# Kernel tuning notes

Measured on AMD Instinct MI355X. Metric: run time of the kernel, lower is better.

Reference implementation:

```python
import jax, jax.numpy as jnp
import numpy as np
import math

N = 50000      # nodes (single node type 'mapping_var')
D = 128        # in_feats
R = 3          # relations
E = 800000     # edges per relation
OUT = 64
ALPHA = 0.5
BETA1 = math.log(2.0)    # log(lambda/layer + 1), layer=1, lambda=1
BETA2 = math.log(1.5)    # layer=2
SLOPE = 0.01             # leaky_relu default negative slope


def setup_inputs() -> dict:
    key = jax.random.key(0)
    ks = jax.random.split(key, 8)
    x = jax.random.normal(ks[0], (N, D), dtype=jnp.float32)
    src = jax.random.randint(ks[1], (R, E), 0, N, dtype=jnp.int32)
    dst = jax.random.randint(ks[2], (R, E), 0, N, dtype=jnp.int32)
    W1 = jax.random.normal(ks[3], (R, D, D), dtype=jnp.float32) * 0.05
    b1 = jnp.zeros((R, D), dtype=jnp.float32)
    W2 = jax.random.normal(ks[4], (R, D, D), dtype=jnp.float32) * 0.05
    b2 = jnp.zeros((R, D), dtype=jnp.float32)
    Wlin = jax.random.normal(ks[5], (D, OUT), dtype=jnp.float32) * 0.05
    blin = jnp.zeros((OUT,), dtype=jnp.float32)
    return {"x": x, "src": src, "dst": dst, "W1": W1, "b1": b1,
            "W2": W2, "b2": b2, "Wlin": Wlin, "blin": blin}


def _gcn2_rel(h, feat0, src, dst, W, b, beta, act):
    """One GCN2Conv on one relation. h,feat0: [N,D]; src,dst: [E]."""
    ones = jnp.ones(src.shape, h.dtype)
    deg_out = jnp.maximum(jax.ops.segment_sum(ones, src, num_segments=N), 1.0)
    deg_in = jnp.maximum(jax.ops.segment_sum(ones, dst, num_segments=N), 1.0)
    hs = h * (deg_out ** -0.5)[:, None]              # src-side normalize
    agg = jax.ops.segment_sum(hs[src], dst, num_segments=N)  # SpMM via gather+scatter
    feat = agg * (deg_in ** -0.5)[:, None]           # dst-side normalize
    rst = feat * (1.0 - ALPHA) + ALPHA * feat0       # initial-residual blend
    rst = (1.0 - beta) * rst + beta * (rst @ W) + b  # identity mapping (project_initial_features)
    if act:
        rst = jnp.where(rst >= 0, rst, SLOPE * rst)  # leaky_relu
    return rst


def reference(x, src, dst, W1, b1, W2, b2, Wlin, blin):
    # conv1: per-relation GCN2Conv(layer=1, leaky_relu), mean-aggregate over relations
    h1 = jax.vmap(lambda s, d, w, bb: _gcn2_rel(x, x, s, d, w, bb, BETA1, True))(
        src, dst, W1, b1).mean(axis=0)
    # dropout: eval-mode identity
    # conv2: per-relation GCN2Conv(layer=2, no activation), feat_0 = original inputs
    h2 = jax.vmap(lambda s, d, w, bb: _gcn2_rel(h1, x, s, d, w, bb, BETA2, False))(
        src, dst, W2, b2).mean(axis=0)
    return h2 @ Wlin + blin
```

## Files before the change

### kernel.cpp

```cpp
#include <hip/hip_runtime.h>

#define NN    50000
#define DD    128
#define RR    3
#define EE    800000
#define OUTD  64
#define BKT   128
#define NBK   391
#define CAP   2560
#define CAPB  2560
#define CHUNK 8192
#define NCH   98
#define NPB   3125
#define SETUPB 6250
#define MCB   49
#define PGB   391
#define P64B  3125
#define ALPHA_ 0.5f
#define SLOPE_ 0.01f
#define BETA1_ 0.6931471805599453f
#define BETA2_ 0.4054651081081644f

typedef __attribute__((ext_vector_type(8))) short short8;
typedef __attribute__((ext_vector_type(4))) float f32x4;
typedef __attribute__((ext_vector_type(4))) unsigned int u32x4;

__device__ __forceinline__ unsigned short f2b(float f) {
    unsigned int u = __builtin_bit_cast(unsigned int, f);
    u += 0x7FFFu + ((u >> 16) & 1u);
    return (unsigned short)(u >> 16);
}
__device__ __forceinline__ unsigned int pack2(float lo, float hi) {
    return (unsigned int)f2b(lo) | ((unsigned int)f2b(hi) << 16);
}
__device__ __forceinline__ float blo(unsigned int w) { return __builtin_bit_cast(float, w << 16); }
__device__ __forceinline__ float bhi(unsigned int w) { return __builtin_bit_cast(float, w & 0xFFFF0000u); }

__global__ __launch_bounds__(256) void bin_kernel(
    const int* __restrict__ src, const int* __restrict__ dst,
    int* __restrict__ bcnt_d, int* __restrict__ bcnt_s,
    int* __restrict__ pairs_d, unsigned short* __restrict__ pairs_s)
{
    __shared__ int hist[NBK];
    __shared__ int lbase[NBK];
    __shared__ int gdelta[NBK];
    __shared__ int lcur[NBK];
    __shared__ unsigned int staging[CHUNK];
    unsigned short* staging16 = (unsigned short*)staging;
    const int tid = threadIdx.x;
    const int blk = blockIdx.x;
    const int phase = (blk >= RR * NCH);
    const int rb = phase ? blk - RR * NCH : blk;
    const int r = rb / NCH;
    const int chunk = rb % NCH;
    const int e0 = chunk * CHUNK;
    const int n = min(CHUNK, EE - e0);
    const int* sp = src + (size_t)r * EE + e0;
    const int* dp = dst + (size_t)r * EE + e0;
    const int* kp = phase ? sp : dp;

    for (int i = tid; i < NBK; i += 256) hist[i] = 0;
    __syncthreads();
    for (int i = tid; i < n; i += 256)
        atomicAdd(&hist[kp[i] >> 7], 1);
    __syncthreads();
    if (tid < 64) {
        int carry = 0;
        for (int c0 = 0; c0 < NBK; c0 += 64) {
            const int idx = c0 + tid;
            const int v = (idx < NBK) ? hist[idx] : 0;
            int incl = v;
            #pragma unroll
            for (int d = 1; d < 64; d <<= 1) {
                const int t = __shfl_up(incl, d, 64);
                if (tid >= d) incl += t;
            }
            if (idx < NBK) lbase[idx] = carry + incl - v;
            carry += __shfl(incl, 63, 64);
        }
    }
    __syncthreads();
    if (!phase) {
        for (int b = tid; b < NBK; b += 256) {
            lcur[b] = lbase[b];
            const int h = hist[b];
            if (h > 0) {
                const int gstart = (r * NBK + b) * CAP + atomicAdd(&bcnt_d[r * NBK + b], h);
                gdelta[b] = gstart - lbase[b];
            }
        }
        __syncthreads();
        for (int i = tid; i < n; i += 256) {
            const int d = dp[i];
            const int b = d >> 7;
            const int pos = atomicAdd(&lcur[b], 1);
            staging[pos] = (unsigned int)sp[i] | ((unsigned int)(d & 127) << 16)
                         | ((unsigned int)b << 23);
        }
        __syncthreads();
        for (int j = tid; j < n; j += 256) {
            const unsigned int v = staging[j];
            const int b = v >> 23;
            const int gi = gdelta[b] + j;
            const int lo = gi - (r * NBK + b) * CAP;
            if (lo < CAP) pairs_d[gi] = (int)(v & 0x7FFFFF);
        }
    } else {
        for (int b = tid; b < NBK; b += 256) {
            lcur[b] = lbase[b];
            const int h = hist[b];
            if (h > 0) {
                const int gstart = (r * NBK + b) * CAPB + atomicAdd(&bcnt_s[r * NBK + b], h);
                gdelta[b] = gstart - lbase[b];
            }
        }
        __syncthreads();
        for (int i = tid; i < n; i += 256) {
            const int s = sp[i];
            const int b = s >> 7;
            const int pos = atomicAdd(&lcur[b], 1);
            staging16[pos] = (unsigned short)((b << 7) | (s & 127));
        }
        __syncthreads();
        for (int j = tid; j < n; j += 256) {
            const unsigned short v = staging16[j];
            const int b = v >> 7;
            const int gi = gdelta[b] + j;
            const int lo = gi - (r * NBK + b) * CAPB;
            if (lo < CAPB) pairs_s[gi] = v;
        }
    }
}

__global__ __launch_bounds__(256) void dego_setup_kernel(
    const unsigned short* __restrict__ pairs_s, const int* __restrict__ bcnt_s,
    float* __restrict__ dego_r,
    const float* __restrict__ x, unsigned short* __restrict__ xb,
    const float* __restrict__ W1, const float* __restrict__ W2,
    const float* __restrict__ Wlin, unsigned short* __restrict__ Wt1,
    unsigned short* __restrict__ Wt2, unsigned short* __restrict__ WlT,
    const float* __restrict__ b2, const float* __restrict__ blin,
    unsigned short* __restrict__ MT, float* __restrict__ Cbuf)
{
    __shared__ int scnt[BKT];
    const int tid = threadIdx.x;
    const int blk = blockIdx.x;
    if (blk < RR * NBK) {
        const int n2 = min(bcnt_s[blk], CAPB);
        const unsigned short* ps = pairs_s + (size_t)blk * CAPB;
        if (tid < BKT) scnt[tid] = 0;
        __syncthreads();
        for (int i = tid; i < n2; i += 256)
            atomicAdd(&scnt[ps[i] & 127], 1);
        __syncthreads();
        if (tid < BKT) {
            const int r = blk / NBK;
            const int g = (blk % NBK) * BKT + tid;
            if (g < NN)
                dego_r[r * NN + g] = rsqrtf((float)max(scnt[tid], 1));
        }
    } else if (blk < RR * NBK + SETUPB) {
        const int i = (blk - RR * NBK) * 256 + tid;
        {
            const float4 v = ((const float4*)x)[i];
            ushort4 o;
            o.x = f2b(v.x); o.y = f2b(v.y); o.z = f2b(v.z); o.w = f2b(v.w);
            ((ushort4*)xb)[i] = o;
        }
        if (i < RR * DD * DD) {
            const int r = i >> 14, rem = i & 16383, nn = rem >> 7, k = rem & 127;
            const float diag = (k == nn) ? 1.0f : 0.0f;
            const float w1 = W1[r * DD * DD + k * DD + nn];
            Wt1[i] = f2b(BETA1_ * w1 + diag * (1.0f - BETA1_));
            const float w2 = W2[r * DD * DD + k * DD + nn];
            Wt2[i] = f2b((BETA2_ * w2 + diag * (1.0f - BETA2_)) * (1.0f / 3.0f));
        } else if (i < RR * DD * DD + OUTD * DD) {
            const int j = i - RR * DD * DD;
            const int nn = j >> 7, k = j & 127;
            WlT[j] = f2b(Wlin[k * OUTD + nn]);
        }
    } else {
        const int mb = blk - RR * NBK - SETUPB;
        if (mb < MCB - 1) {
            const int base = (mb * 256 + tid) * 2;
            #pragma unroll
            for (int ii = 0; ii < 2; ++ii) {
                const int gidx = base + ii;
                const int r = gidx >> 13;
                const int rem = gidx & 8191;
                const int o = rem >> 7, k = rem & 127;
                float s = 0.f;
                for (int nn = 0; nn < DD; ++nn)
                    s += W2[r * DD * DD + k * DD + nn] * Wlin[nn * OUTD + o];
                MT[gidx] = f2b((BETA2_ / 3.0f) * s + ((1.0f - BETA2_) / 3.0f) * Wlin[k * OUTD + o]);
            }
        } else {
            if (tid < OUTD) {
                float s = blin[tid];
                for (int nn = 0; nn < DD; ++nn) {
                    const float mb2 = (b2[nn] + b2[DD + nn] + b2[2 * DD + nn]) * (1.0f / 3.0f);
                    s += mb2 * Wlin[nn * OUTD + tid];
                }
                Cbuf[tid] = s;
            }
        }
    }
}

__global__ __launch_bounds__(256) void sort_kernel(
    int* __restrict__ pairs_d, const int* __restrict__ bcnt_d,
    const float* __restrict__ dego_r,
    int* __restrict__ off_g, int* __restrict__ cnt_g, float* __restrict__ degi_r)
{
    __shared__ int stage[CAP];
    __shared__ int cnt[BKT];
    __shared__ int base[BKT];
    __shared__ int pos[BKT];
    const int tid = threadIdx.x;
    const int bid = blockIdx.x;
    const int rr = bid / NBK;
    const int n = min(bcnt_d[bid], CAP);
    int* pp = pairs_d + (size_t)bid * CAP;
    const float* dego = dego_r + (size_t)rr * NN;
    if (tid < BKT) cnt[tid] = 0;
    __syncthreads();
    for (int i = tid; i < n; i += 256) {
        const int p = pp[i];
        stage[i] = p;
        atomicAdd(&cnt[p >> 16], 1);
    }
    __syncthreads();
    if (tid < 64) {
        int carry = 0;
        for (int c0 = 0; c0 < BKT; c0 += 64) {
            const int v = cnt[c0 + tid];
            int incl = v;
            #pragma unroll
            for (int d = 1; d < 64; d <<= 1) {
                const int t = __shfl_up(incl, d, 64);
                if (tid >= d) incl += t;
            }
            base[c0 + tid] = carry + incl - v;
            carry += __shfl(incl, 63, 64);
        }
    }
    __syncthreads();
    if (tid < BKT) {
        pos[tid] = base[tid];
        const int g = (bid % NBK) * BKT + tid;
        if (g < NN) {
            off_g[rr * NN + g] = bid * CAP + base[tid];
            cnt_g[rr * NN + g] = cnt[tid];
            degi_r[rr * NN + g] = rsqrtf((float)max(cnt[tid], 1));
        }
    }
    __syncthreads();
    for (int i = tid; i < n; i += 256) {
        const int p = stage[i];
        const int q = atomicAdd(&pos[p >> 16], 1);
        const int s = p & 0xFFFF;
        pp[q] = s | ((int)f2b(dego[s]) << 16);
    }
}

__global__ __launch_bounds__(256) void pull_all_kernel(
    const unsigned short* __restrict__ hb,
    const unsigned short* __restrict__ xb,
    const int* __restrict__ csrw, const int* __restrict__ off_g,
    const int* __restrict__ cnt_g, const float* __restrict__ degi_r,
    unsigned short* __restrict__ aggb)
{
    const int blk = blockIdx.x;
    const int r = blk / NPB;
    const int node = (blk % NPB) * 16 + (threadIdx.x >> 4);
    const int lane = threadIdx.x & 15;
    const int gi = r * NN + node;
    const int j0 = off_g[gi];
    const int j1 = j0 + cnt_g[gi];
    const u32x4* hb4 = (const u32x4*)hb;
    float a0 = 0.f, a1 = 0.f, a2 = 0.f, a3 = 0.f, a4 = 0.f, a5 = 0.f, a6 = 0.f, a7 = 0.f;
    int j = j0;
    for (; j + 4 <= j1; j += 4) {
        const unsigned int p0 = csrw[j],     p1 = csrw[j + 1];
        const unsigned int p2 = csrw[j + 2], p3 = csrw[j + 3];
        const float n0 = bhi(p0), n1 = bhi(p1), n2 = bhi(p2), n3 = bhi(p3);
        const u32x4 q0 = hb4[(size_t)(p0 & 0xFFFF) * 16 + lane];
        const u32x4 q1 = hb4[(size_t)(p1 & 0xFFFF) * 16 + lane];
        const u32x4 q2 = hb4[(size_t)(p2 & 0xFFFF) * 16 + lane];
        const u32x4 q3 = hb4[(size_t)(p3 & 0xFFFF) * 16 + lane];
        a0 += blo(q0.x) * n0 + blo(q1.x) * n1 + blo(q2.x) * n2 + blo(q3.x) * n3;
        a1 += bhi(q0.x) * n0 + bhi(q1.x) * n1 + bhi(q2.x) * n2 + bhi(q3.x) * n3;
        a2 += blo(q0.y) * n0 + blo(q1.y) * n1 + blo(q2.y) * n2 + blo(q3.y) * n3;
        a3 += bhi(q0.y) * n0 + bhi(q1.y) * n1 + bhi(q2.y) * n2 + bhi(q3.y) * n3;
        a4 += blo(q0.z) * n0 + blo(q1.z) * n1 + blo(q2.z) * n2 + blo(q3.z) * n3;
        a5 += bhi(q0.z) * n0 + bhi(q1.z) * n1 + bhi(q2.z) * n2 + bhi(q3.z) * n3;
        a6 += blo(q0.w) * n0 + blo(q1.w) * n1 + blo(q2.w) * n2 + blo(q3.w) * n3;
        a7 += bhi(q0.w) * n0 + bhi(q1.w) * n1 + bhi(q2.w) * n2 + bhi(q3.w) * n3;
    }
    for (; j < j1; ++j) {
        const unsigned int p0 = csrw[j];
        const float n0 = bhi(p0);
        const u32x4 q0 = hb4[(size_t)(p0 & 0xFFFF) * 16 + lane];
        a0 += blo(q0.x) * n0; a1 += bhi(q0.x) * n0;
        a2 += blo(q0.y) * n0; a3 += bhi(q0.y) * n0;
        a4 += blo(q0.z) * n0; a5 += bhi(q0.z) * n0;
        a6 += blo(q0.w) * n0; a7 += bhi(q0.w) * n0;
    }
    const float nd = degi_r[gi] * (1.0f - ALPHA_);
    const u32x4 xq = ((const u32x4*)xb)[(size_t)node * 16 + lane];
    u32x4 o;
    o.x = pack2(a0 * nd + ALPHA_ * blo(xq.x), a1 * nd + ALPHA_ * bhi(xq.x));
    o.y = pack2(a2 * nd + ALPHA_ * blo(xq.y), a3 * nd + ALPHA_ * bhi(xq.y));
    o.z = pack2(a4 * nd + ALPHA_ * blo(xq.z), a5 * nd + ALPHA_ * bhi(xq.z));
    o.w = pack2(a6 * nd + ALPHA_ * blo(xq.w), a7 * nd + ALPHA_ * bhi(xq.w));
    ((u32x4*)aggb)[(size_t)gi * 16 + lane] = o;
}

template<int LIN>
__global__ __launch_bounds__(256) void conv_mfma_kernel(
    const unsigned short* __restrict__ aggb,
    const unsigned short* __restrict__ WtG,
    const float* __restrict__ bias,
    const unsigned short* __restrict__ WlT,
    const float* __restrict__ blin,
    unsigned short* __restrict__ houtb,
    float* __restrict__ outf)
{
    __shared__ unsigned short WtL[DD * 136];
    uint4* WtL4 = (uint4*)WtL;
    const int tid  = threadIdx.x;
    const int wave = tid >> 6;
    const int lane = tid & 63;
    const int l15  = lane & 15;
    const int q    = lane >> 4;
    const int blockRow = blockIdx.x * 64;
    const int row0 = blockRow + wave * 16;
    const int arow = min(row0 + l15, NN - 1);

    f32x4 o[8];
    if (LIN) {
        #pragma unroll
        for (int ct = 0; ct < 8; ++ct) {
            const int col = ct * 16 + l15;
            const float bv = (bias[col] + bias[DD + col] + bias[2 * DD + col]) * (1.0f / 3.0f);
            o[ct] = (f32x4){bv, bv, bv, bv};
        }
    } else {
        #pragma unroll
        for (int ct = 0; ct < 8; ++ct) o[ct] = (f32x4){0.f, 0.f, 0.f, 0.f};
    }

    short8 a_cur[4], a_nxt[4];
    {
        const uint4* ap = (const uint4*)aggb + (size_t)arow * 16 + q;
        #pragma unroll
        for (int ks = 0; ks < 4; ++ks)
            a_cur[ks] = __builtin_bit_cast(short8, ap[ks * 4]);
    }

    for (int r = 0; r < RR; ++r) {
        __syncthreads();
        const uint4* wg = (const uint4*)(WtG + (size_t)r * DD * DD);
        for (int i = tid; i < DD * 16; i += 256)
            WtL4[(i >> 4) * 17 + (i & 15)] = wg[i];
        if (r + 1 < RR) {
            const uint4* ap = (const uint4*)aggb + ((size_t)(r + 1) * NN + arow) * 16 + q;
            #pragma unroll
            for (int ks = 0; ks < 4; ++ks)
                a_nxt[ks] = __builtin_bit_cast(short8, ap[ks * 4]);
        }
        __syncthreads();

        #pragma unroll
        for (int ct = 0; ct < 8; ++ct) {
            f32x4 acc;
            if (LIN) {
                acc = o[ct];
            } else {
                const float bv = bias[r * DD + ct * 16 + l15];
                acc = (f32x4){bv, bv, bv, bv};
            }
            const int nrow = ct * 16 + l15;
            #pragma unroll
            for (int ks = 0; ks < 4; ++ks) {
                const short8 b = __builtin_bit_cast(short8, WtL4[nrow * 17 + ks * 4 + q]);
                acc = __builtin_amdgcn_mfma_f32_16x16x32_bf16(a_cur[ks], b, acc, 0, 0, 0);
            }
            if (LIN) {
                o[ct] = acc;
            } else {
                #pragma unroll
                for (int e = 0; e < 4; ++e) {
                    float v = acc[e];
                    v = v >= 0.f ? v : SLOPE_ * v;
                    o[ct][e] += v * (1.0f / 3.0f);
                }
            }
        }
        #pragma unroll
        for (int ks = 0; ks < 4; ++ks) a_cur[ks] = a_nxt[ks];
    }

    __syncthreads();
    unsigned short* tile = WtL;
    #pragma unroll
    for (int ct = 0; ct < 8; ++ct) {
        const int col = ct * 16 + l15;
        #pragma unroll
        for (int e = 0; e < 4; ++e) {
            const int lrow = wave * 16 + q * 4 + e;
            tile[lrow * 136 + col] = f2b(o[ct][e]);
        }
    }
    __syncthreads();
    for (int i = tid; i < 64 * 16; i += 256) {
        const int lrow = i >> 4, c = i & 15;
        const int grow = blockRow + lrow;
        if (grow < NN)
            ((uint4*)houtb)[(size_t)grow * 16 + c] = WtL4[lrow * 17 + c];
    }
}

__global__ __launch_bounds__(512) void pgemm_kernel(
    const unsigned short* __restrict__ h1b,
    const unsigned short* __restrict__ xb,
    const unsigned short* __restrict__ MT,
    unsigned short* __restrict__ Pb,
    unsigned short* __restrict__ Qb)
{
    __shared__ unsigned short MTL[RR * 64 * 136];
    uint4* MTL4 = (uint4*)MTL;
    const int tid  = threadIdx.x;
    const int wave = tid >> 6;
    const int lane = tid & 63;
    const int l15  = lane & 15;
    const int q    = lane >> 4;
    const int blockRow = blockIdx.x * 128;
    const int row0 = blockRow + wave * 16;
    const int arow = min(row0 + l15, NN - 1);

    {
        const uint4* mg = (const uint4*)MT;
        for (int i = tid; i < RR * 64 * 16; i += 512)
            MTL4[(i >> 4) * 17 + (i & 15)] = mg[i];
    }
    short8 ah[4], ax[4];
    {
        const uint4* hp = (const uint4*)h1b + (size_t)arow * 16 + q;
        const uint4* xp = (const uint4*)xb + (size_t)arow * 16 + q;
        #pragma unroll
        for (int ks = 0; ks < 4; ++ks) {
            ah[ks] = __builtin_bit_cast(short8, hp[ks * 4]);
            ax[ks] = __builtin_bit_cast(short8, xp[ks * 4]);
        }
    }
    __syncthreads();

    for (int r = 0; r < RR; ++r) {
        #pragma unroll
        for (int ct = 0; ct < 4; ++ct) {
            f32x4 acc = (f32x4){0.f, 0.f, 0.f, 0.f};
            const int orow = r * 64 + ct * 16 + l15;
            #pragma unroll
            for (int ks = 0; ks < 4; ++ks) {
                const short8 b = __builtin_bit_cast(short8, MTL4[orow * 17 + ks * 4 + q]);
                acc = __builtin_amdgcn_mfma_f32_16x16x32_bf16(ah[ks], b, acc, 0, 0, 0);
            }
            #pragma unroll
            for (int e = 0; e < 4; ++e) {
                const int grow = row0 + q * 4 + e;
                if (grow < NN)
                    Pb[((size_t)r * NN + grow) * OUTD + ct * 16 + l15] = f2b(acc[e]);
            }
        }
    }
    #pragma unroll
    for (int ct = 0; ct < 4; ++ct) {
        f32x4 acc = (f32x4){0.f, 0.f, 0.f, 0.f};
        for (int r = 0; r < RR; ++r) {
            const int orow = r * 64 + ct * 16 + l15;
            #pragma unroll
            for (int ks = 0; ks < 4; ++ks) {
                const short8 b = __builtin_bit_cast(short8, MTL4[orow * 17 + ks * 4 + q]);
                acc = __builtin_amdgcn_mfma_f32_16x16x32_bf16(ax[ks], b, acc, 0, 0, 0);
            }
        }
        #pragma unroll
        for (int e = 0; e < 4; ++e) {
            const int grow = row0 + q * 4 + e;
            if (grow < NN)
                Qb[(size_t)grow * OUTD + ct * 16 + l15] = f2b(acc[e] * ALPHA_);
        }
    }
}

__global__ __launch_bounds__(256) void pull64_kernel(
    const unsigned short* __restrict__ Pb,
    const unsigned short* __restrict__ Qb,
    const float* __restrict__ Cbuf,
    const int* __restrict__ csrw, const int* __restrict__ off_g,
    const int* __restrict__ cnt_g, const float* __restrict__ degi_r,
    float* __restrict__ outf)
{
    const int node = blockIdx.x * 16 + (threadIdx.x >> 4);
    const int lane = threadIdx.x & 15;
    const uint2* P2 = (const uint2*)Pb;
    float t0, t1, t2, t3;
    {
        const uint2 qq = ((const uint2*)Qb)[(size_t)node * 16 + lane];
        const float4 cv = ((const float4*)Cbuf)[lane];
        t0 = blo(qq.x) + cv.x; t1 = bhi(qq.x) + cv.y;
        t2 = blo(qq.y) + cv.z; t3 = bhi(qq.y) + cv.w;
    }
    for (int r = 0; r < RR; ++r) {
        const int gi = r * NN + node;
        const int j0 = off_g[gi];
        const int j1 = j0 + cnt_g[gi];
        const uint2* Pr = P2 + (size_t)r * NN * 16;
        float a0 = 0.f, a1 = 0.f, a2 = 0.f, a3 = 0.f;
        int j = j0;
        for (; j + 4 <= j1; j += 4) {
            const unsigned int p0 = csrw[j],     p1 = csrw[j + 1];
            const unsigned int p2 = csrw[j + 2], p3 = csrw[j + 3];
            const float n0 = bhi(p0), n1 = bhi(p1), n2 = bhi(p2), n3 = bhi(p3);
            const uint2 q0 = Pr[(size_t)(p0 & 0xFFFF) * 16 + lane];
            const uint2 q1 = Pr[(size_t)(p1 & 0xFFFF) * 16 + lane];
            const uint2 q2 = Pr[(size_t)(p2 & 0xFFFF) * 16 + lane];
            const uint2 q3 = Pr[(size_t)(p3 & 0xFFFF) * 16 + lane];
            a0 += blo(q0.x) * n0 + blo(q1.x) * n1 + blo(q2.x) * n2 + blo(q3.x) * n3;
            a1 += bhi(q0.x) * n0 + bhi(q1.x) * n1 + bhi(q2.x) * n2 + bhi(q3.x) * n3;
            a2 += blo(q0.y) * n0 + blo(q1.y) * n1 + blo(q2.y) * n2 + blo(q3.y) * n3;
            a3 += bhi(q0.y) * n0 + bhi(q1.y) * n1 + bhi(q2.y) * n2 + bhi(q3.y) * n3;
        }
        for (; j < j1; ++j) {
            const unsigned int p0 = csrw[j];
            const float n0 = bhi(p0);
            const uint2 q0 = Pr[(size_t)(p0 & 0xFFFF) * 16 + lane];
            a0 += blo(q0.x) * n0; a1 += bhi(q0.x) * n0;
            a2 += blo(q0.y) * n0; a3 += bhi(q0.y) * n0;
        }
        const float nd = degi_r[gi] * (1.0f - ALPHA_);
        t0 += a0 * nd; t1 += a1 * nd; t2 += a2 * nd; t3 += a3 * nd;
    }
    float4 ov; ov.x = t0; ov.y = t1; ov.z = t2; ov.w = t3;
    ((float4*)outf)[(size_t)node * 16 + lane] = ov;
}

extern "C" void kernel_launch(void* const* d_in, const int* in_sizes, int n_in,
                              void* d_out, int out_size, void* d_ws, size_t ws_size,
                              hipStream_t stream)
{
    const float* x    = (const float*)d_in[0];
    const int*   src  = (const int*)  d_in[1];
    const int*   dst  = (const int*)  d_in[2];
    const float* W1   = (const float*)d_in[3];
    const float* b1   = (const float*)d_in[4];
    const float* W2   = (const float*)d_in[5];
    const float* b2   = (const float*)d_in[6];
    const float* Wlin = (const float*)d_in[7];
    const float* blin = (const float*)d_in[8];
    float* out = (float*)d_out;

    int*   bcnt_d  = (int*)d_ws;
    int*   bcnt_s  = bcnt_d + RR * NBK;
    float* dego_r  = (float*)(bcnt_s + RR * NBK);
    float* degi_r  = dego_r + RR * NN;
    int*   off_g   = (int*)(degi_r + RR * NN);
    int*   cnt_g   = off_g + RR * NN;
    int*   pairs_d = cnt_g + RR * NN + 2;
    unsigned short* pairs_s = (unsigned short*)(pairs_d + (size_t)RR * NBK * CAP);
    unsigned short* xb   = pairs_s + (size_t)RR * NBK * CAPB;
    unsigned short* h1b  = xb + (size_t)NN * DD;
    unsigned short* aggb = h1b + (size_t)NN * DD;
    unsigned short* Wt1  = aggb + (size_t)RR * NN * DD;
    unsigned short* Wt2  = Wt1 + RR * DD * DD;
    unsigned short* WlT  = Wt2 + RR * DD * DD;
    unsigned short* MT   = WlT + OUTD * DD;
    float*          Cbuf = (float*)(MT + RR * DD * OUTD);
    unsigned short* Pb = aggb;
    unsigned short* Qb = aggb + (size_t)RR * NN * OUTD;

    hipMemsetAsync(bcnt_d, 0, (size_t)2 * RR * NBK * sizeof(int), stream);

    const int gemm_blocks = (NN + 63) / 64;

    bin_kernel<<<2 * RR * NCH, 256, 0, stream>>>(src, dst, bcnt_d, bcnt_s, pairs_d, pairs_s);
    dego_setup_kernel<<<RR * NBK + SETUPB + MCB, 256, 0, stream>>>(
        pairs_s, bcnt_s, dego_r, x, xb, W1, W2, Wlin, Wt1, Wt2, WlT, b2, blin, MT, Cbuf);
    sort_kernel<<<RR * NBK, 256, 0, stream>>>(
        pairs_d, bcnt_d, dego_r, off_g, cnt_g, degi_r);

    pull_all_kernel<<<RR * NPB, 256, 0, stream>>>(
        xb, xb, pairs_d, off_g, cnt_g, degi_r, aggb);
    conv_mfma_kernel<0><<<gemm_blocks, 256, 0, stream>>>(
        aggb, Wt1, b1, nullptr, nullptr, h1b, nullptr);

    pgemm_kernel<<<PGB, 512, 0, stream>>>(h1b, xb, MT, Pb, Qb);
    pull64_kernel<<<P64B, 256, 0, stream>>>(
        Pb, Qb, Cbuf, pairs_d, off_g, cnt_g, degi_r, out);
}
```

Before: 376.5 us.

## Merge binning, out-degree and setup into one prep kernel with direct degree histograms

Folds the edge binning, out-degree computation and weight/feature casting into a single 1024-thread prep kernel, so one launch and one dependency boundary go away. Out-degrees are now counted directly with packed 16-bit shared-memory histograms, one block per relation over all edges, which replaces the separate source-side binning pass and its pairs buffer. It also removes the unused linear-head path from the conv kernel. The risk is that three single blocks each scanning 800K edges become a serial tail, and 1024-thread blocks with about 100KB of shared memory limit occupancy for the binning blocks.

```diff
diff --git a/kernel.cpp b/kernel.cpp
--- a/kernel.cpp
+++ b/kernel.cpp
@@ -11,9 +11,10 @@
 #define CAPB  2560
 #define CHUNK 8192
 #define NCH   98
+#define NBINA (RR * NCH)
+#define DEGB  RR
+#define CASTB 1563
 #define NPB   3125
-#define SETUPB 6250
-#define MCB   49
 #define PGB   391
 #define P64B  3125
 #define ALPHA_ 0.5f
@@ -36,132 +37,96 @@
 __device__ __forceinline__ float blo(unsigned int w) { return __builtin_bit_cast(float, w << 16); }
 __device__ __forceinline__ float bhi(unsigned int w) { return __builtin_bit_cast(float, w & 0xFFFF0000u); }
 
-__global__ __launch_bounds__(256) void bin_kernel(
+__global__ __launch_bounds__(1024, 1) void prep_kernel(
     const int* __restrict__ src, const int* __restrict__ dst,
-    int* __restrict__ bcnt_d, int* __restrict__ bcnt_s,
-    int* __restrict__ pairs_d, unsigned short* __restrict__ pairs_s)
-{
-    __shared__ int hist[NBK];
-    __shared__ int lbase[NBK];
-    __shared__ int gdelta[NBK];
-    __shared__ int lcur[NBK];
-    __shared__ unsigned int staging[CHUNK];
-    unsigned short* staging16 = (unsigned short*)staging;
-    const int tid = threadIdx.x;
-    const int blk = blockIdx.x;
-    const int phase = (blk >= RR * NCH);
-    const int rb = phase ? blk - RR * NCH : blk;
-    const int r = rb / NCH;
-    const int chunk = rb % NCH;
-    const int e0 = chunk * CHUNK;
-    const int n = min(CHUNK, EE - e0);
-    const int* sp = src + (size_t)r * EE + e0;
-    const int* dp = dst + (size_t)r * EE + e0;
-    const int* kp = phase ? sp : dp;
-
-    for (int i = tid; i < NBK; i += 256) hist[i] = 0;
-    __syncthreads();
-    for (int i = tid; i < n; i += 256)
-        atomicAdd(&hist[kp[i] >> 7], 1);
-    __syncthreads();
-    if (tid < 64) {
-        int carry = 0;
-        for (int c0 = 0; c0 < NBK; c0 += 64) {
-            const int idx = c0 + tid;
-            const int v = (idx < NBK) ? hist[idx] : 0;
-            int incl = v;
-            #pragma unroll
-            for (int d = 1; d < 64; d <<= 1) {
-                const int t = __shfl_up(incl, d, 64);
-                if (tid >= d) incl += t;
-            }
-            if (idx < NBK) lbase[idx] = carry + incl - v;
-            carry += __shfl(incl, 63, 64);
-        }
-    }
-    __syncthreads();
-    if (!phase) {
-        for (int b = tid; b < NBK; b += 256) {
-            lcur[b] = lbase[b];
-            const int h = hist[b];
-            if (h > 0) {
-                const int gstart = (r * NBK + b) * CAP + atomicAdd(&bcnt_d[r * NBK + b], h);
-                gdelta[b] = gstart - lbase[b];
-            }
-        }
-        __syncthreads();
-        for (int i = tid; i < n; i += 256) {
-            const int d = dp[i];
-            const int b = d >> 7;
-            const int pos = atomicAdd(&lcur[b], 1);
-            staging[pos] = (unsigned int)sp[i] | ((unsigned int)(d & 127) << 16)
-                         | ((unsigned int)b << 23);
-        }
-        __syncthreads();
-        for (int j = tid; j < n; j += 256) {
-            const unsigned int v = staging[j];
-            const int b = v >> 23;
-            const int gi = gdelta[b] + j;
-            const int lo = gi - (r * NBK + b) * CAP;
-            if (lo < CAP) pairs_d[gi] = (int)(v & 0x7FFFFF);
-        }
-    } else {
-        for (int b = tid; b < NBK; b += 256) {
-            lcur[b] = lbase[b];
-            const int h = hist[b];
-            if (h > 0) {
-                const int gstart = (r * NBK + b) * CAPB + atomicAdd(&bcnt_s[r * NBK + b], h);
-                gdelta[b] = gstart - lbase[b];
-            }
-        }
-        __syncthreads();
-        for (int i = tid; i < n; i += 256) {
-            const int s = sp[i];
-            const int b = s >> 7;
-            const int pos = atomicAdd(&lcur[b], 1);
-            staging16[pos] = (unsigned short)((b << 7) | (s & 127));
-        }
-        __syncthreads();
-        for (int j = tid; j < n; j += 256) {
-            const unsigned short v = staging16[j];
-            const int b = v >> 7;
-            const int gi = gdelta[b] + j;
-            const int lo = gi - (r * NBK + b) * CAPB;
-            if (lo < CAPB) pairs_s[gi] = v;
-        }
-    }
-}
-
-__global__ __launch_bounds__(256) void dego_setup_kernel(
-    const unsigned short* __restrict__ pairs_s, const int* __restrict__ bcnt_s,
+    int* __restrict__ bcnt_d, int* __restrict__ pairs_d,
     float* __restrict__ dego_r,
     const float* __restrict__ x, unsigned short* __restrict__ xb,
     const float* __restrict__ W1, const float* __restrict__ W2,
     const float* __restrict__ Wlin, unsigned short* __restrict__ Wt1,
-    unsigned short* __restrict__ Wt2, unsigned short* __restrict__ WlT,
+    unsigned short* __restrict__ Wt2,
     const float* __restrict__ b2, const float* __restrict__ blin,
     unsigned short* __restrict__ MT, float* __restrict__ Cbuf)
 {
-    __shared__ int scnt[BKT];
+    __shared__ unsigned int shmem[25000];
     const int tid = threadIdx.x;
     const int blk = blockIdx.x;
-    if (blk < RR * NBK) {
-        const int n2 = min(bcnt_s[blk], CAPB);
-        const unsigned short* ps = pairs_s + (size_t)blk * CAPB;
-        if (tid < BKT) scnt[tid] = 0;
-        __syncthreads();
-        for (int i = tid; i < n2; i += 256)
-            atomicAdd(&scnt[ps[i] & 127], 1);
-        __syncthreads();
-        if (tid < BKT) {
-            const int r = blk / NBK;
-            const int g = (blk % NBK) * BKT + tid;
-            if (g < NN)
-                dego_r[r * NN + g] = rsqrtf((float)max(scnt[tid], 1));
-        }
-    } else if (blk < RR * NBK + SETUPB) {
-        const int i = (blk - RR * NBK) * 256 + tid;
-        {
+
+    if (blk < NBINA) {
+        unsigned int* hist   = shmem;
+        unsigned int* lbase  = shmem + NBK;
+        unsigned int* gdelta = shmem + 2 * NBK;
+        unsigned int* lcur   = shmem + 3 * NBK;
+        unsigned int* staging = shmem + 4 * NBK;
+        const int r = blk / NCH;
+        const int chunk = blk % NCH;
+        const int e0 = chunk * CHUNK;
+        const int n = min(CHUNK, EE - e0);
+        const int* sp = src + (size_t)r * EE + e0;
+        const int* dp = dst + (size_t)r * EE + e0;
+
+        for (int i = tid; i < NBK; i += 1024) hist[i] = 0;
+        __syncthreads();
+        for (int i = tid; i < n; i += 1024)
+            atomicAdd(&hist[dp[i] >> 7], 1u);
+        __syncthreads();
+        if (tid < 64) {
+            int carry = 0;
+            for (int c0 = 0; c0 < NBK; c0 += 64) {
+                const int idx = c0 + tid;
+                const int v = (idx < NBK) ? (int)hist[idx] : 0;
+                int incl = v;
+                #pragma unroll
+                for (int d = 1; d < 64; d <<= 1) {
+                    const int t = __shfl_up(incl, d, 64);
+                    if (tid >= d) incl += t;
+                }
+                if (idx < NBK) lbase[idx] = carry + incl - v;
+                carry += __shfl(incl, 63, 64);
+            }
+        }
+        __syncthreads();
+        for (int b = tid; b < NBK; b += 1024) {
+            lcur[b] = lbase[b];
+            const int h = (int)hist[b];
+            if (h > 0) {
+                const int gstart = (r * NBK + b) * CAP + atomicAdd(&bcnt_d[r * NBK + b], h);
+                gdelta[b] = (unsigned int)(gstart - (int)lbase[b]);
+            }
+        }
+        __syncthreads();
+        for (int i = tid; i < n; i += 1024) {
+            const int d = dp[i];
+            const int b = d >> 7;
+            const int pos = atomicAdd(&lcur[b], 1u);
+            staging[pos] = (unsigned int)sp[i] | ((unsigned int)(d & 127) << 16)
+                         | ((unsigned int)b << 23);
+        }
+        __syncthreads();
+        for (int j = tid; j < n; j += 1024) {
+            const unsigned int v = staging[j];
+            const int b = v >> 23;
+            const int gi = (int)gdelta[b] + j;
+            const int lo = gi - (r * NBK + b) * CAP;
+            if (lo < CAP) pairs_d[gi] = (int)(v & 0x7FFFFF);
+        }
+    } else if (blk < NBINA + DEGB) {
+        const int r = blk - NBINA;
+        for (int i = tid; i < 25000; i += 1024) shmem[i] = 0;
+        __syncthreads();
+        const int* sp = src + (size_t)r * EE;
+        for (int e = tid; e < EE; e += 1024) {
+            const int s = sp[e];
+            atomicAdd(&shmem[s >> 1], 1u << ((s & 1) * 16));
+        }
+        __syncthreads();
+        for (int g = tid; g < NN; g += 1024) {
+            const int cnt = (int)((shmem[g >> 1] >> ((g & 1) * 16)) & 0xFFFFu);
+            dego_r[r * NN + g] = rsqrtf((float)max(cnt, 1));
+        }
+    } else {
+        const int i = (blk - NBINA - DEGB) * 1024 + tid;
+        if (i < NN * DD / 4) {
             const float4 v = ((const float4*)x)[i];
             ushort4 o;
             o.x = f2b(v.x); o.y = f2b(v.y); o.z = f2b(v.z); o.w = f2b(v.w);
@@ -174,35 +139,23 @@
             Wt1[i] = f2b(BETA1_ * w1 + diag * (1.0f - BETA1_));
             const float w2 = W2[r * DD * DD + k * DD + nn];
             Wt2[i] = f2b((BETA2_ * w2 + diag * (1.0f - BETA2_)) * (1.0f / 3.0f));
-        } else if (i < RR * DD * DD + OUTD * DD) {
-            const int j = i - RR * DD * DD;
-            const int nn = j >> 7, k = j & 127;
-            WlT[j] = f2b(Wlin[k * OUTD + nn]);
-        }
-    } else {
-        const int mb = blk - RR * NBK - SETUPB;
-        if (mb < MCB - 1) {
-            const int base = (mb * 256 + tid) * 2;
-            #pragma unroll
-            for (int ii = 0; ii < 2; ++ii) {
-                const int gidx = base + ii;
-                const int r = gidx >> 13;
-                const int rem = gidx & 8191;
-                const int o = rem >> 7, k = rem & 127;
-                float s = 0.f;
-                for (int nn = 0; nn < DD; ++nn)
-                    s += W2[r * DD * DD + k * DD + nn] * Wlin[nn * OUTD + o];
-                MT[gidx] = f2b((BETA2_ / 3.0f) * s + ((1.0f - BETA2_) / 3.0f) * Wlin[k * OUTD + o]);
-            }
-        } else {
-            if (tid < OUTD) {
-                float s = blin[tid];
-                for (int nn = 0; nn < DD; ++nn) {
-                    const float mb2 = (b2[nn] + b2[DD + nn] + b2[2 * DD + nn]) * (1.0f / 3.0f);
-                    s += mb2 * Wlin[nn * OUTD + tid];
-                }
-                Cbuf[tid] = s;
-            }
+        }
+        if (i < RR * OUTD * DD) {
+            const int r = i >> 13;
+            const int rem = i & 8191;
+            const int o = rem >> 7, k = rem & 127;
+            float s = 0.f;
+            for (int nn = 0; nn < DD; ++nn)
+                s += W2[r * DD * DD + k * DD + nn] * Wlin[nn * OUTD + o];
+            MT[i] = f2b((BETA2_ / 3.0f) * s + ((1.0f - BETA2_) / 3.0f) * Wlin[k * OUTD + o]);
+        }
+        if (i < OUTD) {
+            float s = blin[i];
+            for (int nn = 0; nn < DD; ++nn) {
+                const float mb2 = (b2[nn] + b2[DD + nn] + b2[2 * DD + nn]) * (1.0f / 3.0f);
+                s += mb2 * Wlin[nn * OUTD + i];
+            }
+            Cbuf[i] = s;
         }
     }
 }
@@ -321,10 +274,7 @@
     const unsigned short* __restrict__ aggb,
     const unsigned short* __restrict__ WtG,
     const float* __restrict__ bias,
-    const unsigned short* __restrict__ WlT,
-    const float* __restrict__ blin,
-    unsigned short* __restrict__ houtb,
-    float* __restrict__ outf)
+    unsigned short* __restrict__ houtb)
 {
     __shared__ unsigned short WtL[DD * 136];
     uint4* WtL4 = (uint4*)WtL;
@@ -338,17 +288,8 @@
     const int arow = min(row0 + l15, NN - 1);
 
     f32x4 o[8];
-    if (LIN) {
-        #pragma unroll
-        for (int ct = 0; ct < 8; ++ct) {
-            const int col = ct * 16 + l15;
-            const float bv = (bias[col] + bias[DD + col] + bias[2 * DD + col]) * (1.0f / 3.0f);
-            o[ct] = (f32x4){bv, bv, bv, bv};
-        }
-    } else {
-        #pragma unroll
-        for (int ct = 0; ct < 8; ++ct) o[ct] = (f32x4){0.f, 0.f, 0.f, 0.f};
-    }
+    #pragma unroll
+    for (int ct = 0; ct < 8; ++ct) o[ct] = (f32x4){0.f, 0.f, 0.f, 0.f};
 
     short8 a_cur[4], a_nxt[4];
     {
@@ -373,28 +314,19 @@
 
         #pragma unroll
         for (int ct = 0; ct < 8; ++ct) {
-            f32x4 acc;
-            if (LIN) {
-                acc = o[ct];
-            } else {
-                const float bv = bias[r * DD + ct * 16 + l15];
-                acc = (f32x4){bv, bv, bv, bv};
-            }
+            const float bv = bias[r * DD + ct * 16 + l15];
+            f32x4 acc = (f32x4){bv, bv, bv, bv};
             const int nrow = ct * 16 + l15;
             #pragma unroll
             for (int ks = 0; ks < 4; ++ks) {
                 const short8 b = __builtin_bit_cast(short8, WtL4[nrow * 17 + ks * 4 + q]);
                 acc = __builtin_amdgcn_mfma_f32_16x16x32_bf16(a_cur[ks], b, acc, 0, 0, 0);
             }
-            if (LIN) {
-                o[ct] = acc;
-            } else {
-                #pragma unroll
-                for (int e = 0; e < 4; ++e) {
-                    float v = acc[e];
-                    v = v >= 0.f ? v : SLOPE_ * v;
-                    o[ct][e] += v * (1.0f / 3.0f);
-                }
+            #pragma unroll
+            for (int e = 0; e < 4; ++e) {
+                float v = acc[e];
+                v = v >= 0.f ? v : SLOPE_ * v;
+                o[ct][e] += v * (1.0f / 3.0f);
             }
         }
         #pragma unroll
@@ -580,20 +512,20 @@
     unsigned short* Pb = aggb;
     unsigned short* Qb = aggb + (size_t)RR * NN * OUTD;
 
-    hipMemsetAsync(bcnt_d, 0, (size_t)2 * RR * NBK * sizeof(int), stream);
+    hipMemsetAsync(bcnt_d, 0, (size_t)RR * NBK * sizeof(int), stream);
 
     const int gemm_blocks = (NN + 63) / 64;
 
-    bin_kernel<<<2 * RR * NCH, 256, 0, stream>>>(src, dst, bcnt_d, bcnt_s, pairs_d, pairs_s);
-    dego_setup_kernel<<<RR * NBK + SETUPB + MCB, 256, 0, stream>>>(
-        pairs_s, bcnt_s, dego_r, x, xb, W1, W2, Wlin, Wt1, Wt2, WlT, b2, blin, MT, Cbuf);
+    prep_kernel<<<NBINA + DEGB + CASTB, 1024, 0, stream>>>(
+        src, dst, bcnt_d, pairs_d, dego_r, x, xb, W1, W2, Wlin, Wt1, Wt2,
+        b2, blin, MT, Cbuf);
     sort_kernel<<<RR * NBK, 256, 0, stream>>>(
         pairs_d, bcnt_d, dego_r, off_g, cnt_g, degi_r);
 
     pull_all_kernel<<<RR * NPB, 256, 0, stream>>>(
         xb, xb, pairs_d, off_g, cnt_g, degi_r, aggb);
     conv_mfma_kernel<0><<<gemm_blocks, 256, 0, stream>>>(
-        aggb, Wt1, b1, nullptr, nullptr, h1b, nullptr);
+        aggb, Wt1, b1, h1b);
 
     pgemm_kernel<<<PGB, 512, 0, stream>>>(h1b, xb, MT, Pb, Qb);
     pull64_kernel<<<P64B, 256, 0, stream>>>(
```

Result: slower. 566.1 us (+50.3%).
